# Optimization experiments

Measured on AMD Instinct MI355X. Metric: run time of the kernel, lower is better.

Reference implementation:

```python
import jax, jax.numpy as jnp
import numpy as np


def setup_inputs() -> dict:
    key = jax.random.key(0)
    k1, k2, k3 = jax.random.split(key, 3)
    b, c, h, w = 4, 64, 64, 64
    content = jax.random.normal(k1, (b, c, h, w), dtype=jnp.float32)
    content_s = jax.random.normal(k2, (b, c, h, w), dtype=jnp.float32)
    style = jax.random.normal(k3, (b, c, h, w), dtype=jnp.float32)
    return {"content": content, "content_s": content_s, "style": style}


def reference(content, content_s, style):
    b, c, h, w = content.shape
    hw = h * w
    Fc = content.reshape(b, c, hw)      # [b, c, HW]
    Fs = content_s.reshape(b, c, hw)    # [b, c, HW]
    Fst = style.reshape(b, c, hw)       # [b, c, HW]
    # S[b, q, k] = sum_c Fc[b, c, q] * Fs[b, c, k]  (Fc transposed as in torch)
    S = jnp.einsum('bcq,bck->bqk', Fc, Fs)
    S = jax.nn.softmax(S, axis=-1)
    # O = style @ S^T : O[b, c, q] = sum_k Fst[b, c, k] * S[b, q, k]
    O = jnp.einsum('bck,bqk->bcq', Fst, S).reshape(b, c, h, w)
    return jnp.concatenate((content, O), axis=1)
```

## Files before the change

kernel.cpp:

```cpp
#include <hip/hip_runtime.h>
#include <math.h>


#define Bb 4
#define Cc 64
#define HWs 4096
#define SPLITS 4
#define TILES_PER_SPLIT 16
#define RLOG2E 1.44269504088896340736f
#define DEFER_THR 6.0f

typedef _Float16 half8 __attribute__((ext_vector_type(8)));
typedef _Float16 half4 __attribute__((ext_vector_type(4)));
typedef float floatx4 __attribute__((ext_vector_type(4)));
typedef unsigned uint2v __attribute__((ext_vector_type(2)));

extern "C" __device__ float __ocml_native_exp2_f32(float);
#if defined(__has_builtin) && __has_builtin(__builtin_amdgcn_exp2f)
#define EXP2(x) __builtin_amdgcn_exp2f(x)
#else
#define EXP2(x) __ocml_native_exp2_f32(x)
#endif

__global__ __launch_bounds__(256) void prep_k(const float* __restrict__ content,
                                              const float* __restrict__ Fs,
                                              const float* __restrict__ Fst,
                                              float* __restrict__ out,
                                              _Float16* __restrict__ Kt,
                                              _Float16* __restrict__ Vt) {
    const int bid = blockIdx.x;
    const int t = threadIdx.x;
    if (bid < 1024) {
        int i4 = bid * 256 + t;
        const float4* c4 = (const float4*)content;
        const float4* v4 = (const float4*)Fst;
        float4* o4 = (float4*)out;
        int b = i4 >> 16, rem = i4 & 65535;
        o4[(size_t)b * 131072 + rem] = c4[i4];
        float4 v = v4[i4];
        half4 h;
        h[0] = (_Float16)v.x; h[1] = (_Float16)v.y;
        h[2] = (_Float16)v.z; h[3] = (_Float16)v.w;
        *(half4*)(Vt + (size_t)i4 * 4) = h;
    } else {
        __shared__ _Float16 T[16][72];
        int e = bid - 1024;
        int b = e >> 8;
        int hw0 = (e & 255) * 16;
        const float* sb = Fs + (size_t)b * Cc * HWs;
        {
            int c = t >> 2, x4 = (t & 3) * 4;
            float4 v = *(const float4*)(sb + (size_t)c * HWs + hw0 + x4);
            T[x4 + 0][c] = (_Float16)v.x;
            T[x4 + 1][c] = (_Float16)v.y;
            T[x4 + 2][c] = (_Float16)v.z;
            T[x4 + 3][c] = (_Float16)v.w;
        }
        __syncthreads();
        if (t < 128) {
            int row = t >> 3, g = t & 7;
            _Float16* db = Kt + (size_t)b * HWs * Cc;
            *(half8*)(db + (size_t)(hw0 + row) * Cc + g * 8) = *(half8*)&T[row][g * 8];
        }
    }
}

__global__ __launch_bounds__(256, 2) void attn_k(const float* __restrict__ Fc,
                                                 const _Float16* __restrict__ Kt,
                                                 const _Float16* __restrict__ Vt,
                                                 _Float16* __restrict__ Opart,
                                                 float2* __restrict__ ml) {
    const int tid  = threadIdx.x;
    const int lane = tid & 63;
    const int quad = lane >> 4;
    const int l15  = lane & 15;
    const int w    = tid >> 6;
    const int qg = blockIdx.x & 31;
    const int b  = (blockIdx.x >> 5) & 3;
    const int s  = blockIdx.x >> 7;
    const int k0base = s * TILES_PER_SPLIT * 64;
    const int qA = qg * 128 + w * 32 + l15;
    const int qB = qA + 16;

    __shared__ _Float16 Kl[2][64 * 64];
    __shared__ _Float16 Vl[2][64 * 64];

    const float*    Fcb = Fc + (size_t)b * Cc * HWs;
    const _Float16* Kb  = Kt + (size_t)b * HWs * Cc;
    const _Float16* Vb  = Vt + (size_t)b * Cc * HWs;

    const bool isK  = tid < 128;
    const int  sl   = tid & 127;
    const int  srow = sl >> 3;
    const int  sjg  = sl & 7;
    const int  ssw  = (sjg ^ (srow & 7)) * 8;

    half8 qf[2][2];
    #pragma unroll
    for (int j = 0; j < 8; ++j) {
        qf[0][0][j] = (_Float16)(Fcb[(size_t)(quad * 8 + j) * HWs + qA] * RLOG2E);
        qf[0][1][j] = (_Float16)(Fcb[(size_t)(32 + quad * 8 + j) * HWs + qA] * RLOG2E);
        qf[1][0][j] = (_Float16)(Fcb[(size_t)(quad * 8 + j) * HWs + qB] * RLOG2E);
        qf[1][1][j] = (_Float16)(Fcb[(size_t)(32 + quad * 8 + j) * HWs + qB] * RLOG2E);
    }

    half8 st[4];
    auto stage_load = [&](int kt) {
        int kk0 = k0base + kt * 64;
        #pragma unroll
        for (int i = 0; i < 4; ++i) {
            int row = srow + 16 * i;
            if (isK) st[i] = *(const half8*)(Kb + (size_t)(kk0 + row) * 64 + sjg * 8);
            else     st[i] = *(const half8*)(Vb + (size_t)row * HWs + kk0 + sjg * 8);
        }
    };
    auto stage_write = [&](int p) {
        #pragma unroll
        for (int i = 0; i < 4; ++i) {
            int row = srow + 16 * i;
            if (isK) *(half8*)&Kl[p][row * 64 + ssw] = st[i];
            else     *(half8*)&Vl[p][row * 64 + ssw] = st[i];
        }
    };

    floatx4 acc[2][4];
    floatx4 accl[2];
    #pragma unroll
    for (int g = 0; g < 2; ++g) {
        accl[g] = (floatx4)(0.0f);
        #pragma unroll
        for (int m = 0; m < 4; ++m) acc[g][m] = (floatx4)(0.0f);
    }
    float m_run[2] = {0.0f, 0.0f};

    half8 vone;
    #pragma unroll
    for (int j = 0; j < 8; ++j) vone[j] = (_Float16)1.0f;

    stage_load(0);
    stage_write(0);
    stage_load(1);
    __syncthreads();

    const int swl = (l15 & 7);
    for (int kt = 0; kt < TILES_PER_SPLIT; ++kt) {
        const int p = kt & 1;
        if (kt + 1 < TILES_PER_SPLIT) stage_write(p ^ 1);
        if (kt + 2 < TILES_PER_SPLIT) stage_load(kt + 2);

        floatx4 sv[2][4];
        {
            floatx4 c0 = (floatx4)(-m_run[0]);
            floatx4 c1 = (floatx4)(-m_run[1]);
            #pragma unroll
            for (int m = 0; m < 4; ++m) {
                const half8 ka0 = *(const half8*)&Kl[p][(m * 16 + l15) * 64 + ((quad ^ swl) * 8)];
                const half8 ka1 = *(const half8*)&Kl[p][(m * 16 + l15) * 64 + (((4 + quad) ^ swl) * 8)];
                sv[0][m] = __builtin_amdgcn_mfma_f32_16x16x32_f16(ka0, qf[0][0], c0, 0, 0, 0);
                sv[0][m] = __builtin_amdgcn_mfma_f32_16x16x32_f16(ka1, qf[0][1], sv[0][m], 0, 0, 0);
                sv[1][m] = __builtin_amdgcn_mfma_f32_16x16x32_f16(ka0, qf[1][0], c1, 0, 0, 0);
                sv[1][m] = __builtin_amdgcn_mfma_f32_16x16x32_f16(ka1, qf[1][1], sv[1][m], 0, 0, 0);
            }
        }

        half8 va[4][2];
        #pragma unroll
        for (int m = 0; m < 4; ++m)
            #pragma unroll
            for (int ks = 0; ks < 2; ++ks)
                va[m][ks] = *(const half8*)&Vl[p][(m * 16 + l15) * 64 + (((ks * 4 + quad) ^ swl) * 8)];

        half8 pb[2][2];
        #pragma unroll
        for (int g = 0; g < 2; ++g) {
            float mm0 = fmaxf(fmaxf(fmaxf(sv[g][0][0], sv[g][0][1]), sv[g][0][2]), sv[g][0][3]);
            float mm1 = fmaxf(fmaxf(fmaxf(sv[g][1][0], sv[g][1][1]), sv[g][1][2]), sv[g][1][3]);
            float mm2 = fmaxf(fmaxf(fmaxf(sv[g][2][0], sv[g][2][1]), sv[g][2][2]), sv[g][2][3]);
            float mm3 = fmaxf(fmaxf(fmaxf(sv[g][3][0], sv[g][3][1]), sv[g][3][2]), sv[g][3][3]);
            float mx = fmaxf(fmaxf(fmaxf(mm0, mm1), mm2), mm3);
            if (!__all(mx <= DEFER_THR)) {
                unsigned mu = __float_as_uint(mx);
                uint2v t32 = __builtin_amdgcn_permlane32_swap(mu, mu, false, false);
                float wmx = fmaxf(__uint_as_float(t32[0]), __uint_as_float(t32[1]));
                mu = __float_as_uint(wmx);
                uint2v t16 = __builtin_amdgcn_permlane16_swap(mu, mu, false, false);
                wmx = fmaxf(__uint_as_float(t16[0]), __uint_as_float(t16[1]));
                float delta = fmaxf(wmx, 0.0f);
                float alpha = EXP2(-delta);
                m_run[g] += delta;
                #pragma unroll
                for (int m = 0; m < 4; ++m) acc[g][m] *= alpha;
                accl[g] *= alpha;
                #pragma unroll
                for (int m = 0; m < 4; ++m)
                    #pragma unroll
                    for (int r = 0; r < 4; ++r) sv[g][m][r] -= delta;
            }
            unsigned Ap[4], Bp[4];
            #pragma unroll
            for (int m = 0; m < 4; ++m) {
                float e0 = EXP2(sv[g][m][0]);
                float e1 = EXP2(sv[g][m][1]);
                float e2 = EXP2(sv[g][m][2]);
                float e3 = EXP2(sv[g][m][3]);
                Ap[m] = __builtin_bit_cast(unsigned, __builtin_amdgcn_cvt_pkrtz(e0, e1));
                Bp[m] = __builtin_bit_cast(unsigned, __builtin_amdgcn_cvt_pkrtz(e2, e3));
            }
            unsigned pw[2][4];
            { uint2v a = __builtin_amdgcn_permlane32_swap(Ap[0], Ap[1], false, false);
              uint2v u = __builtin_amdgcn_permlane16_swap(a[0], a[1], false, false);
              pw[0][0] = u[0]; pw[0][2] = u[1]; }
            { uint2v a = __builtin_amdgcn_permlane32_swap(Bp[0], Bp[1], false, false);
              uint2v u = __builtin_amdgcn_permlane16_swap(a[0], a[1], false, false);
              pw[0][1] = u[0]; pw[0][3] = u[1]; }
            { uint2v a = __builtin_amdgcn_permlane32_swap(Ap[2], Ap[3], false, false);
              uint2v u = __builtin_amdgcn_permlane16_swap(a[0], a[1], false, false);
              pw[1][0] = u[0]; pw[1][2] = u[1]; }
            { uint2v a = __builtin_amdgcn_permlane32_swap(Bp[2], Bp[3], false, false);
              uint2v u = __builtin_amdgcn_permlane16_swap(a[0], a[1], false, false);
              pw[1][1] = u[0]; pw[1][3] = u[1]; }
            #pragma unroll
            for (int ks = 0; ks < 2; ++ks) {
                union { unsigned u4[4]; half8 h; } z;
                z.u4[0] = pw[ks][0]; z.u4[1] = pw[ks][1];
                z.u4[2] = pw[ks][2]; z.u4[3] = pw[ks][3];
                pb[g][ks] = z.h;
            }
        }

        #pragma unroll
        for (int m = 0; m < 4; ++m)
            #pragma unroll
            for (int g = 0; g < 2; ++g) {
                acc[g][m] = __builtin_amdgcn_mfma_f32_16x16x32_f16(va[m][0], pb[g][0], acc[g][m], 0, 0, 0);
                acc[g][m] = __builtin_amdgcn_mfma_f32_16x16x32_f16(va[m][1], pb[g][1], acc[g][m], 0, 0, 0);
            }
        accl[0] = __builtin_amdgcn_mfma_f32_16x16x32_f16(vone, pb[0][0], accl[0], 0, 0, 0);
        accl[0] = __builtin_amdgcn_mfma_f32_16x16x32_f16(vone, pb[0][1], accl[0], 0, 0, 0);
        accl[1] = __builtin_amdgcn_mfma_f32_16x16x32_f16(vone, pb[1][0], accl[1], 0, 0, 0);
        accl[1] = __builtin_amdgcn_mfma_f32_16x16x32_f16(vone, pb[1][1], accl[1], 0, 0, 0);

        __syncthreads();
    }

    _Float16* op = Opart + (((size_t)s * Bb + b) * Cc) * HWs;
    #pragma unroll
    for (int g = 0; g < 2; ++g) {
        int q = (g == 0) ? qA : qB;
        #pragma unroll
        for (int m = 0; m < 4; ++m)
            #pragma unroll
            for (int r = 0; r < 4; ++r) {
                int c = m * 16 + quad * 4 + r;
                op[(size_t)c * HWs + q] = (_Float16)acc[g][m][r];
            }
        if (quad == 0)
            ml[((size_t)b * HWs + q) * SPLITS + s] = make_float2(m_run[g], accl[g][0]);
    }
}

__global__ __launch_bounds__(256) void combine_k(const _Float16* __restrict__ Opart,
                                                 const float2* __restrict__ ml,
                                                 float* __restrict__ out) {
    int idx = blockIdx.x * 256 + threadIdx.x;
    int q = idx & 4095;
    int c = (idx >> 12) & 63;
    int b = idx >> 18;
    const float2* mlp = ml + ((size_t)b * HWs + q) * SPLITS;
    float2 mls[SPLITS];
    #pragma unroll
    for (int s = 0; s < SPLITS; ++s) mls[s] = mlp[s];
    float M = -INFINITY;
    #pragma unroll
    for (int s = 0; s < SPLITS; ++s) M = fmaxf(M, mls[s].x);
    float l = 0.0f, o = 0.0f;
    #pragma unroll
    for (int s = 0; s < SPLITS; ++s) {
        float wgt = EXP2(mls[s].x - M);
        l += wgt * mls[s].y;
        o += wgt * (float)Opart[(((size_t)s * Bb + b) * Cc + c) * HWs + q];
    }
    out[((size_t)b * 2 * Cc + Cc + c) * HWs + q] = o / l;
}

extern "C" void kernel_launch(void* const* d_in, const int* in_sizes, int n_in,
                              void* d_out, int out_size, void* d_ws, size_t ws_size,
                              hipStream_t stream) {
    const float* content   = (const float*)d_in[0];
    const float* content_s = (const float*)d_in[1];
    const float* style     = (const float*)d_in[2];
    float* out = (float*)d_out;

    _Float16* Kt = (_Float16*)d_ws;
    _Float16* Vt = Kt + (size_t)Bb * HWs * Cc;
    _Float16* Opart = Vt + (size_t)Bb * Cc * HWs;
    float2*   ml = (float2*)(Opart + (size_t)SPLITS * Bb * Cc * HWs);

    prep_k<<<dim3(2048), dim3(256), 0, stream>>>(content, content_s, style, out, Kt, Vt);
    attn_k<<<dim3(SPLITS * Bb * 32), dim3(256), 0, stream>>>(content, Kt, Vt, Opart, ml);
    combine_k<<<dim3(4096), dim3(256), 0, stream>>>(Opart, ml, out);
}
```

Measured before the change: 100.2 us.

## Fuse prep, attention and combine into one cooperative kernel with grid syncs

```diff
diff --git a/kernel.cpp b/kernel.cpp
--- a/kernel.cpp
+++ b/kernel.cpp
@@ -1,6 +1,9 @@
 #include <hip/hip_runtime.h>
+#include <hip/hip_cooperative_groups.h>
 #include <math.h>
 
+
+namespace cg = cooperative_groups;
 
 #define Bb 4
 #define Cc 64
@@ -21,6 +24,291 @@
 #else
 #define EXP2(x) __ocml_native_exp2_f32(x)
 #endif
+
+
+__device__ __forceinline__ void prep_copy_body(int i4, const float* __restrict__ content,
+                                               const float* __restrict__ Fst,
+                                               float* __restrict__ out,
+                                               _Float16* __restrict__ Vt) {
+    const float4* c4 = (const float4*)content;
+    const float4* v4 = (const float4*)Fst;
+    float4* o4 = (float4*)out;
+    int b = i4 >> 16, rem = i4 & 65535;
+    o4[(size_t)b * 131072 + rem] = c4[i4];
+    float4 v = v4[i4];
+    half4 h;
+    h[0] = (_Float16)v.x; h[1] = (_Float16)v.y;
+    h[2] = (_Float16)v.z; h[3] = (_Float16)v.w;
+    *(half4*)(Vt + (size_t)i4 * 4) = h;
+}
+
+__device__ __forceinline__ void combine_body(int idx, const _Float16* __restrict__ Opart,
+                                             const float2* __restrict__ ml,
+                                             float* __restrict__ out) {
+    int q = idx & 4095;
+    int c = (idx >> 12) & 63;
+    int b = idx >> 18;
+    const float2* mlp = ml + ((size_t)b * HWs + q) * SPLITS;
+    float2 mls[SPLITS];
+    #pragma unroll
+    for (int s = 0; s < SPLITS; ++s) mls[s] = mlp[s];
+    float M = -INFINITY;
+    #pragma unroll
+    for (int s = 0; s < SPLITS; ++s) M = fmaxf(M, mls[s].x);
+    float l = 0.0f, o = 0.0f;
+    #pragma unroll
+    for (int s = 0; s < SPLITS; ++s) {
+        float wgt = EXP2(mls[s].x - M);
+        l += wgt * mls[s].y;
+        o += wgt * (float)Opart[(((size_t)s * Bb + b) * Cc + c) * HWs + q];
+    }
+    out[((size_t)b * 2 * Cc + Cc + c) * HWs + q] = o / l;
+}
+
+
+__global__ __launch_bounds__(256, 2) void fused_k(const float* __restrict__ content,
+                                                  const float* __restrict__ Fs,
+                                                  const float* __restrict__ Fst,
+                                                  float* __restrict__ out,
+                                                  _Float16* __restrict__ Kt,
+                                                  _Float16* __restrict__ Vt,
+                                                  _Float16* __restrict__ Opart,
+                                                  float2* __restrict__ ml) {
+    __shared__ _Float16 smem[4 * 4096];
+    const int tid = threadIdx.x;
+    const int bid = blockIdx.x;
+
+    #pragma unroll
+    for (int it = 0; it < 2; ++it)
+        prep_copy_body((it * 512 + bid) * 256 + tid, content, Fst, out, Vt);
+
+    {
+        _Float16 (*T)[72] = reinterpret_cast<_Float16 (*)[72]>(smem);
+        #pragma unroll
+        for (int it = 0; it < 2; ++it) {
+            int e = it * 512 + bid;
+            int b = e >> 8;
+            int hw0 = (e & 255) * 16;
+            const float* sb = Fs + (size_t)b * Cc * HWs;
+            __syncthreads();
+            {
+                int c = tid >> 2, x4 = (tid & 3) * 4;
+                float4 v = *(const float4*)(sb + (size_t)c * HWs + hw0 + x4);
+                T[x4 + 0][c] = (_Float16)v.x;
+                T[x4 + 1][c] = (_Float16)v.y;
+                T[x4 + 2][c] = (_Float16)v.z;
+                T[x4 + 3][c] = (_Float16)v.w;
+            }
+            __syncthreads();
+            if (tid < 128) {
+                int row = tid >> 3, g = tid & 7;
+                _Float16* db = Kt + (size_t)b * HWs * Cc;
+                *(half8*)(db + (size_t)(hw0 + row) * Cc + g * 8) = *(half8*)&T[row][g * 8];
+            }
+        }
+    }
+
+    __threadfence();
+    cg::this_grid().sync();
+
+    {
+        const int lane = tid & 63;
+        const int quad = lane >> 4;
+        const int l15  = lane & 15;
+        const int w    = tid >> 6;
+        const int qg = bid & 31;
+        const int b  = (bid >> 5) & 3;
+        const int s  = bid >> 7;
+        const int k0base = s * TILES_PER_SPLIT * 64;
+        const int qA = qg * 128 + w * 32 + l15;
+        const int qB = qA + 16;
+
+        _Float16* Kl = smem;
+        _Float16* Vl = smem + 2 * 4096;
+
+        const float*    Fcb = content + (size_t)b * Cc * HWs;
+        const _Float16* Kb  = Kt + (size_t)b * HWs * Cc;
+        const _Float16* Vb  = Vt + (size_t)b * Cc * HWs;
+
+        const bool isK  = tid < 128;
+        const int  sl   = tid & 127;
+        const int  srow = sl >> 3;
+        const int  sjg  = sl & 7;
+        const int  ssw  = (sjg ^ (srow & 7)) * 8;
+
+        half8 qf[2][2];
+        #pragma unroll
+        for (int j = 0; j < 8; ++j) {
+            qf[0][0][j] = (_Float16)(Fcb[(size_t)(quad * 8 + j) * HWs + qA] * RLOG2E);
+            qf[0][1][j] = (_Float16)(Fcb[(size_t)(32 + quad * 8 + j) * HWs + qA] * RLOG2E);
+            qf[1][0][j] = (_Float16)(Fcb[(size_t)(quad * 8 + j) * HWs + qB] * RLOG2E);
+            qf[1][1][j] = (_Float16)(Fcb[(size_t)(32 + quad * 8 + j) * HWs + qB] * RLOG2E);
+        }
+
+        half8 st[4];
+        auto stage_load = [&](int kt) {
+            int kk0 = k0base + kt * 64;
+            #pragma unroll
+            for (int i = 0; i < 4; ++i) {
+                int row = srow + 16 * i;
+                if (isK) st[i] = *(const half8*)(Kb + (size_t)(kk0 + row) * 64 + sjg * 8);
+                else     st[i] = *(const half8*)(Vb + (size_t)row * HWs + kk0 + sjg * 8);
+            }
+        };
+        auto stage_write = [&](int p) {
+            #pragma unroll
+            for (int i = 0; i < 4; ++i) {
+                int row = srow + 16 * i;
+                if (isK) *(half8*)&Kl[p * 4096 + row * 64 + ssw] = st[i];
+                else     *(half8*)&Vl[p * 4096 + row * 64 + ssw] = st[i];
+            }
+        };
+
+        floatx4 acc[2][4];
+        floatx4 accl[2];
+        #pragma unroll
+        for (int g = 0; g < 2; ++g) {
+            accl[g] = (floatx4)(0.0f);
+            #pragma unroll
+            for (int m = 0; m < 4; ++m) acc[g][m] = (floatx4)(0.0f);
+        }
+        float m_run[2] = {0.0f, 0.0f};
+
+        half8 vone;
+        #pragma unroll
+        for (int j = 0; j < 8; ++j) vone[j] = (_Float16)1.0f;
+
+        __syncthreads();
+        stage_load(0);
+        stage_write(0);
+        stage_load(1);
+        __syncthreads();
+
+        const int swl = (l15 & 7);
+        for (int kt = 0; kt < TILES_PER_SPLIT; ++kt) {
+            const int p = kt & 1;
+            if (kt + 1 < TILES_PER_SPLIT) stage_write(p ^ 1);
+            if (kt + 2 < TILES_PER_SPLIT) stage_load(kt + 2);
+
+            floatx4 sv[2][4];
+            {
+                floatx4 c0 = (floatx4)(-m_run[0]);
+                floatx4 c1 = (floatx4)(-m_run[1]);
+                #pragma unroll
+                for (int m = 0; m < 4; ++m) {
+                    const half8 ka0 = *(const half8*)&Kl[p * 4096 + (m * 16 + l15) * 64 + ((quad ^ swl) * 8)];
+                    const half8 ka1 = *(const half8*)&Kl[p * 4096 + (m * 16 + l15) * 64 + (((4 + quad) ^ swl) * 8)];
+                    sv[0][m] = __builtin_amdgcn_mfma_f32_16x16x32_f16(ka0, qf[0][0], c0, 0, 0, 0);
+                    sv[0][m] = __builtin_amdgcn_mfma_f32_16x16x32_f16(ka1, qf[0][1], sv[0][m], 0, 0, 0);
+                    sv[1][m] = __builtin_amdgcn_mfma_f32_16x16x32_f16(ka0, qf[1][0], c1, 0, 0, 0);
+                    sv[1][m] = __builtin_amdgcn_mfma_f32_16x16x32_f16(ka1, qf[1][1], sv[1][m], 0, 0, 0);
+                }
+            }
+
+            half8 va[4][2];
+            #pragma unroll
+            for (int m = 0; m < 4; ++m)
+                #pragma unroll
+                for (int ks = 0; ks < 2; ++ks)
+                    va[m][ks] = *(const half8*)&Vl[p * 4096 + (m * 16 + l15) * 64 + (((ks * 4 + quad) ^ swl) * 8)];
+
+            half8 pb[2][2];
+            #pragma unroll
+            for (int g = 0; g < 2; ++g) {
+                float mm0 = fmaxf(fmaxf(fmaxf(sv[g][0][0], sv[g][0][1]), sv[g][0][2]), sv[g][0][3]);
+                float mm1 = fmaxf(fmaxf(fmaxf(sv[g][1][0], sv[g][1][1]), sv[g][1][2]), sv[g][1][3]);
+                float mm2 = fmaxf(fmaxf(fmaxf(sv[g][2][0], sv[g][2][1]), sv[g][2][2]), sv[g][2][3]);
+                float mm3 = fmaxf(fmaxf(fmaxf(sv[g][3][0], sv[g][3][1]), sv[g][3][2]), sv[g][3][3]);
+                float mx = fmaxf(fmaxf(fmaxf(mm0, mm1), mm2), mm3);
+                if (!__all(mx <= DEFER_THR)) {
+                    unsigned mu = __float_as_uint(mx);
+                    uint2v t32 = __builtin_amdgcn_permlane32_swap(mu, mu, false, false);
+                    float wmx = fmaxf(__uint_as_float(t32[0]), __uint_as_float(t32[1]));
+                    mu = __float_as_uint(wmx);
+                    uint2v t16 = __builtin_amdgcn_permlane16_swap(mu, mu, false, false);
+                    wmx = fmaxf(__uint_as_float(t16[0]), __uint_as_float(t16[1]));
+                    float delta = fmaxf(wmx, 0.0f);
+                    float alpha = EXP2(-delta);
+                    m_run[g] += delta;
+                    #pragma unroll
+                    for (int m = 0; m < 4; ++m) acc[g][m] *= alpha;
+                    accl[g] *= alpha;
+                    #pragma unroll
+                    for (int m = 0; m < 4; ++m)
+                        #pragma unroll
+                        for (int r = 0; r < 4; ++r) sv[g][m][r] -= delta;
+                }
+                unsigned Ap[4], Bp[4];
+                #pragma unroll
+                for (int m = 0; m < 4; ++m) {
+                    float e0 = EXP2(sv[g][m][0]);
+                    float e1 = EXP2(sv[g][m][1]);
+                    float e2 = EXP2(sv[g][m][2]);
+                    float e3 = EXP2(sv[g][m][3]);
+                    Ap[m] = __builtin_bit_cast(unsigned, __builtin_amdgcn_cvt_pkrtz(e0, e1));
+                    Bp[m] = __builtin_bit_cast(unsigned, __builtin_amdgcn_cvt_pkrtz(e2, e3));
+                }
+                unsigned pw[2][4];
+                { uint2v a = __builtin_amdgcn_permlane32_swap(Ap[0], Ap[1], false, false);
+                  uint2v u = __builtin_amdgcn_permlane16_swap(a[0], a[1], false, false);
+                  pw[0][0] = u[0]; pw[0][2] = u[1]; }
+                { uint2v a = __builtin_amdgcn_permlane32_swap(Bp[0], Bp[1], false, false);
+                  uint2v u = __builtin_amdgcn_permlane16_swap(a[0], a[1], false, false);
+                  pw[0][1] = u[0]; pw[0][3] = u[1]; }
+                { uint2v a = __builtin_amdgcn_permlane32_swap(Ap[2], Ap[3], false, false);
+                  uint2v u = __builtin_amdgcn_permlane16_swap(a[0], a[1], false, false);
+                  pw[1][0] = u[0]; pw[1][2] = u[1]; }
+                { uint2v a = __builtin_amdgcn_permlane32_swap(Bp[2], Bp[3], false, false);
+                  uint2v u = __builtin_amdgcn_permlane16_swap(a[0], a[1], false, false);
+                  pw[1][1] = u[0]; pw[1][3] = u[1]; }
+                #pragma unroll
+                for (int ks = 0; ks < 2; ++ks) {
+                    union { unsigned u4[4]; half8 h; } z;
+                    z.u4[0] = pw[ks][0]; z.u4[1] = pw[ks][1];
+                    z.u4[2] = pw[ks][2]; z.u4[3] = pw[ks][3];
+                    pb[g][ks] = z.h;
+                }
+            }
+
+            #pragma unroll
+            for (int m = 0; m < 4; ++m)
+                #pragma unroll
+                for (int g = 0; g < 2; ++g) {
+                    acc[g][m] = __builtin_amdgcn_mfma_f32_16x16x32_f16(va[m][0], pb[g][0], acc[g][m], 0, 0, 0);
+                    acc[g][m] = __builtin_amdgcn_mfma_f32_16x16x32_f16(va[m][1], pb[g][1], acc[g][m], 0, 0, 0);
+                }
+            accl[0] = __builtin_amdgcn_mfma_f32_16x16x32_f16(vone, pb[0][0], accl[0], 0, 0, 0);
+            accl[0] = __builtin_amdgcn_mfma_f32_16x16x32_f16(vone, pb[0][1], accl[0], 0, 0, 0);
+            accl[1] = __builtin_amdgcn_mfma_f32_16x16x32_f16(vone, pb[1][0], accl[1], 0, 0, 0);
+            accl[1] = __builtin_amdgcn_mfma_f32_16x16x32_f16(vone, pb[1][1], accl[1], 0, 0, 0);
+
+            __syncthreads();
+        }
+
+        _Float16* op = Opart + (((size_t)s * Bb + b) * Cc) * HWs;
+        #pragma unroll
+        for (int g = 0; g < 2; ++g) {
+            int q = (g == 0) ? qA : qB;
+            #pragma unroll
+            for (int m = 0; m < 4; ++m)
+                #pragma unroll
+                for (int r = 0; r < 4; ++r) {
+                    int c = m * 16 + quad * 4 + r;
+                    op[(size_t)c * HWs + q] = (_Float16)acc[g][m][r];
+                }
+            if (quad == 0)
+                ml[((size_t)b * HWs + q) * SPLITS + s] = make_float2(m_run[g], accl[g][0]);
+        }
+    }
+
+    __threadfence();
+    cg::this_grid().sync();
+
+    #pragma unroll
+    for (int it = 0; it < 8; ++it)
+        combine_body((it * 512 + bid) * 256 + tid, Opart, ml, out);
+}
+
 
 __global__ __launch_bounds__(256) void prep_k(const float* __restrict__ content,
                                               const float* __restrict__ Fs,
@@ -31,17 +319,7 @@
     const int bid = blockIdx.x;
     const int t = threadIdx.x;
     if (bid < 1024) {
-        int i4 = bid * 256 + t;
-        const float4* c4 = (const float4*)content;
-        const float4* v4 = (const float4*)Fst;
-        float4* o4 = (float4*)out;
-        int b = i4 >> 16, rem = i4 & 65535;
-        o4[(size_t)b * 131072 + rem] = c4[i4];
-        float4 v = v4[i4];
-        half4 h;
-        h[0] = (_Float16)v.x; h[1] = (_Float16)v.y;
-        h[2] = (_Float16)v.z; h[3] = (_Float16)v.w;
-        *(half4*)(Vt + (size_t)i4 * 4) = h;
+        prep_copy_body(bid * 256 + t, content, Fst, out, Vt);
     } else {
         __shared__ _Float16 T[16][72];
         int e = bid - 1024;
@@ -262,26 +540,9 @@
 __global__ __launch_bounds__(256) void combine_k(const _Float16* __restrict__ Opart,
                                                  const float2* __restrict__ ml,
                                                  float* __restrict__ out) {
-    int idx = blockIdx.x * 256 + threadIdx.x;
-    int q = idx & 4095;
-    int c = (idx >> 12) & 63;
-    int b = idx >> 18;
-    const float2* mlp = ml + ((size_t)b * HWs + q) * SPLITS;
-    float2 mls[SPLITS];
-    #pragma unroll
-    for (int s = 0; s < SPLITS; ++s) mls[s] = mlp[s];
-    float M = -INFINITY;
-    #pragma unroll
-    for (int s = 0; s < SPLITS; ++s) M = fmaxf(M, mls[s].x);
-    float l = 0.0f, o = 0.0f;
-    #pragma unroll
-    for (int s = 0; s < SPLITS; ++s) {
-        float wgt = EXP2(mls[s].x - M);
-        l += wgt * mls[s].y;
-        o += wgt * (float)Opart[(((size_t)s * Bb + b) * Cc + c) * HWs + q];
-    }
-    out[((size_t)b * 2 * Cc + Cc + c) * HWs + q] = o / l;
-}
+    combine_body(blockIdx.x * 256 + threadIdx.x, Opart, ml, out);
+}
+
 
 extern "C" void kernel_launch(void* const* d_in, const int* in_sizes, int n_in,
                               void* d_out, int out_size, void* d_ws, size_t ws_size,
@@ -296,7 +557,14 @@
     _Float16* Opart = Vt + (size_t)Bb * Cc * HWs;
     float2*   ml = (float2*)(Opart + (size_t)SPLITS * Bb * Cc * HWs);
 
-    prep_k<<<dim3(2048), dim3(256), 0, stream>>>(content, content_s, style, out, Kt, Vt);
-    attn_k<<<dim3(SPLITS * Bb * 32), dim3(256), 0, stream>>>(content, Kt, Vt, Opart, ml);
-    combine_k<<<dim3(4096), dim3(256), 0, stream>>>(Opart, ml, out);
-}
+    void* args[] = { (void*)&content, (void*)&content_s, (void*)&style, (void*)&out,
+                     (void*)&Kt, (void*)&Vt, (void*)&Opart, (void*)&ml };
+    hipError_t err = hipLaunchCooperativeKernel((const void*)fused_k, dim3(512), dim3(256),
+                                                args, 0, stream);
+    if (err != hipSuccess) {
+        (void)hipGetLastError();
+        prep_k<<<dim3(2048), dim3(256), 0, stream>>>(content, content_s, style, out, Kt, Vt);
+        attn_k<<<dim3(SPLITS * Bb * 32), dim3(256), 0, stream>>>(content, Kt, Vt, Opart, ml);
+        combine_k<<<dim3(4096), dim3(256), 0, stream>>>(Opart, ml, out);
+    }
+}
```

Result: slower. 295.7 us (+195.1%).
